# Kernel tuning notes

Hardware: AMD Instinct MI355X
Metric: run time of the kernel (lower is better)

Reference implementation:

```python
import jax, jax.numpy as jnp
import numpy as np


def setup_inputs() -> dict:
    key = jax.random.key(0)
    k1, k2 = jax.random.split(key)
    enc_output = jax.random.normal(k1, (4, 4096, 1024), dtype=jnp.float32)
    dec_output = jax.random.normal(k2, (4, 4096, 1024), dtype=jnp.float32)
    return {"enc_output": enc_output, "dec_output": dec_output}


def reference(enc_output, dec_output):
    # a_t[b, e, t] = sum_d enc[b, e, d] * dec[b, t, d]   -> [B, T_enc, T_dec]
    a_t = jnp.einsum('bed,btd->bet', enc_output, dec_output)
    # softmax over dim=1 (the T_enc axis), no scaling, no mask (faithful to source)
    a_t = jax.nn.softmax(a_t, axis=1)
    # c_t[b, t, d] = sum_e a_t[b, e, t] * enc[b, e, d]   -> [B, T_dec, D]
    c_t = jnp.einsum('bet,bed->btd', a_t, enc_output)
    return c_t
```

## Files before the change

kernel.cpp:

```cpp
#include <hip/hip_runtime.h>
#include <hip/hip_fp16.h>

typedef _Float16 half_t;
typedef _Float16 f16x8 __attribute__((ext_vector_type(8)));
typedef _Float16 f16x4 __attribute__((ext_vector_type(4)));
typedef float f32x4 __attribute__((ext_vector_type(4)));

#define SEQ 4096
#define DDIM 1024
#define NBATCH 4

__device__ __forceinline__ void gload16(const half_t* g, half_t* l) {
  __builtin_amdgcn_global_load_lds((const __attribute__((address_space(1))) void*)g,
                                   (__attribute__((address_space(3))) void*)l, 16, 0, 0);
}

__global__ __launch_bounds__(256) void conv_f16(const float* __restrict__ src,
                                                half_t* __restrict__ dst) {
  int i = blockIdx.x * 256 + threadIdx.x;
  float4 x = ((const float4*)src)[i];
  f16x4 o = {(half_t)x.x, (half_t)x.y, (half_t)x.z, (half_t)x.w};
  *(f16x4*)(dst + (size_t)i * 4) = o;
}

__global__ __launch_bounds__(256) void transpose_f16(const float* __restrict__ src,
                                                     half_t* __restrict__ dst) {
  __shared__ float tile[32][33];
  int b = blockIdx.z;
  int e0 = blockIdx.x * 32, d0 = blockIdx.y * 32;
  const float* s = src + (size_t)b * SEQ * DDIM;
  half_t* dt = dst + (size_t)b * DDIM * SEQ;
  int tx = threadIdx.x & 31, ty = threadIdx.x >> 5;
#pragma unroll
  for (int i = 0; i < 4; i++) {
    int e = e0 + ty + i * 8;
    tile[ty + i * 8][tx] = s[(size_t)e * DDIM + d0 + tx];
  }
  __syncthreads();
#pragma unroll
  for (int i = 0; i < 4; i++) {
    int d = d0 + ty + i * 8;
    dt[(size_t)d * SEQ + e0 + tx] = (half_t)tile[tx][ty + i * 8];
  }
}

#define BM 128
#define BN 128
#define BK 64

__global__ __launch_bounds__(256) void gemm_f16(const half_t* __restrict__ A,
                                                const half_t* __restrict__ B,
                                                float* __restrict__ C, int M, int N, int K) {
  __shared__ __align__(16) half_t As[BM * BK];
  __shared__ __align__(16) half_t Bs[BN * BK];
  const int tid = threadIdx.x;
  const int bm = blockIdx.x, bn = blockIdx.y;
  const int wave = tid >> 6, lane = tid & 63;
  const int wm = (wave & 1) * 64, wn = (wave >> 1) * 64;
  const int mrow = lane & 15, quad = lane >> 4;

  f32x4 acc[4][4];
#pragma unroll
  for (int i = 0; i < 4; i++)
#pragma unroll
    for (int j = 0; j < 4; j++) acc[i][j] = {0.f, 0.f, 0.f, 0.f};

  const half_t* Ag = A + (size_t)(bm * BM) * K;
  const half_t* Bg = B + (size_t)(bn * BN) * K;

  for (int k0 = 0; k0 < K; k0 += BK) {
#pragma unroll
    for (int i = 0; i < 4; i++) {
      int cid = i * 256 + tid;
      int row = cid >> 3, slot = cid & 7;
      int chunk = slot ^ (row & 7);
      gload16(Ag + (size_t)row * K + k0 + chunk * 8, &As[row * BK + slot * 8]);
      gload16(Bg + (size_t)row * K + k0 + chunk * 8, &Bs[row * BK + slot * 8]);
    }
    __builtin_amdgcn_s_waitcnt(0);
    __syncthreads();
#pragma unroll
    for (int ks = 0; ks < 2; ks++) {
      f16x8 af[4], bf[4];
#pragma unroll
      for (int i = 0; i < 4; i++) {
        int ra = wm + i * 16 + mrow;
        int rb = wn + i * 16 + mrow;
        int sa = (ks * 4 + quad) ^ (ra & 7);
        int sb = (ks * 4 + quad) ^ (rb & 7);
        af[i] = *(const f16x8*)(&As[ra * BK + sa * 8]);
        bf[i] = *(const f16x8*)(&Bs[rb * BK + sb * 8]);
      }
#pragma unroll
      for (int mi = 0; mi < 4; mi++)
#pragma unroll
        for (int ni = 0; ni < 4; ni++)
          acc[mi][ni] =
              __builtin_amdgcn_mfma_f32_16x16x32_f16(af[mi], bf[ni], acc[mi][ni], 0, 0, 0);
    }
    __syncthreads();
  }
#pragma unroll
  for (int mi = 0; mi < 4; mi++) {
#pragma unroll
    for (int ni = 0; ni < 4; ni++) {
      int row0 = bm * BM + wm + mi * 16 + quad * 4;
      int col = bn * BN + wn + ni * 16 + mrow;
      float* Cp = C + (size_t)row0 * N + col;
#pragma unroll
      for (int r = 0; r < 4; r++) Cp[(size_t)r * N] = acc[mi][ni][r];
    }
  }
}

__global__ __launch_bounds__(256) void softmax_rows(const float* __restrict__ S,
                                                    half_t* __restrict__ P) {
  const int row = blockIdx.x;
  const float4* Sr = (const float4*)(S + (size_t)row * SEQ);
  const int tid = threadIdx.x, lane = tid & 63, wave = tid >> 6;
  __shared__ float red[4];
  __shared__ float bc;
  float4 v[4];
  float m = -1e30f;
#pragma unroll
  for (int j = 0; j < 4; j++) {
    v[j] = Sr[tid + j * 256];
    m = fmaxf(m, fmaxf(fmaxf(v[j].x, v[j].y), fmaxf(v[j].z, v[j].w)));
  }
#pragma unroll
  for (int o = 32; o; o >>= 1) m = fmaxf(m, __shfl_xor(m, o));
  if (lane == 0) red[wave] = m;
  __syncthreads();
  if (tid == 0) bc = fmaxf(fmaxf(red[0], red[1]), fmaxf(red[2], red[3]));
  __syncthreads();
  m = bc;
  float s = 0.f;
#pragma unroll
  for (int j = 0; j < 4; j++) {
    v[j].x = __expf(v[j].x - m);
    v[j].y = __expf(v[j].y - m);
    v[j].z = __expf(v[j].z - m);
    v[j].w = __expf(v[j].w - m);
    s += v[j].x + v[j].y + v[j].z + v[j].w;
  }
#pragma unroll
  for (int o = 32; o; o >>= 1) s += __shfl_xor(s, o);
  __syncthreads();
  if (lane == 0) red[wave] = s;
  __syncthreads();
  if (tid == 0) bc = red[0] + red[1] + red[2] + red[3];
  __syncthreads();
  float r = 1.0f / bc;
  f16x4* Pr = (f16x4*)(P + (size_t)row * SEQ);
#pragma unroll
  for (int j = 0; j < 4; j++) {
    f16x4 o = {(half_t)(v[j].x * r), (half_t)(v[j].y * r), (half_t)(v[j].z * r),
               (half_t)(v[j].w * r)};
    Pr[tid + j * 256] = o;
  }
}

__global__ __launch_bounds__(256) void naive_attn(const float* __restrict__ enc,
                                                  const float* __restrict__ dec,
                                                  float* __restrict__ out) {
  const int b = blockIdx.y, t = blockIdx.x;
  const float* encb = enc + (size_t)b * SEQ * DDIM;
  const float* q = dec + ((size_t)b * SEQ + t) * DDIM;
  __shared__ float qs[DDIM];
  __shared__ float sc[SEQ];
  __shared__ float red[4];
  __shared__ float bc;
  const int tid = threadIdx.x, lane = tid & 63, wave = tid >> 6;
  for (int i = tid; i < DDIM; i += 256) qs[i] = q[i];
  __syncthreads();
  for (int e = tid; e < SEQ; e += 256) {
    const float* er = encb + (size_t)e * DDIM;
    float s = 0.f;
    for (int d = 0; d < DDIM; d += 4) {
      float4 ev = *(const float4*)(er + d);
      s += ev.x * qs[d] + ev.y * qs[d + 1] + ev.z * qs[d + 2] + ev.w * qs[d + 3];
    }
    sc[e] = s;
  }
  __syncthreads();
  float m = -1e30f;
  for (int e = tid; e < SEQ; e += 256) m = fmaxf(m, sc[e]);
#pragma unroll
  for (int o = 32; o; o >>= 1) m = fmaxf(m, __shfl_xor(m, o));
  if (lane == 0) red[wave] = m;
  __syncthreads();
  if (tid == 0) bc = fmaxf(fmaxf(red[0], red[1]), fmaxf(red[2], red[3]));
  __syncthreads();
  m = bc;
  float s = 0.f;
  for (int e = tid; e < SEQ; e += 256) {
    float p = __expf(sc[e] - m);
    sc[e] = p;
    s += p;
  }
#pragma unroll
  for (int o = 32; o; o >>= 1) s += __shfl_xor(s, o);
  __syncthreads();
  if (lane == 0) red[wave] = s;
  __syncthreads();
  if (tid == 0) bc = red[0] + red[1] + red[2] + red[3];
  __syncthreads();
  const float rinv = 1.0f / bc;
  const int d0 = tid * 4;
  float4 acc = {0.f, 0.f, 0.f, 0.f};
  for (int e = 0; e < SEQ; e++) {
    float p = sc[e];
    float4 ev = *(const float4*)(encb + (size_t)e * DDIM + d0);
    acc.x += p * ev.x;
    acc.y += p * ev.y;
    acc.z += p * ev.z;
    acc.w += p * ev.w;
  }
  float4* o4 = (float4*)(out + ((size_t)b * SEQ + t) * DDIM + d0);
  float4 res = {acc.x * rinv, acc.y * rinv, acc.z * rinv, acc.w * rinv};
  *o4 = res;
}

extern "C" void kernel_launch(void* const* d_in, const int* in_sizes, int n_in, void* d_out,
                              int out_size, void* d_ws, size_t ws_size, hipStream_t stream) {
  const float* enc = (const float*)d_in[0];
  const float* dec = (const float*)d_in[1];
  float* out = (float*)d_out;

  const size_t SZ_S = (size_t)SEQ * SEQ * 4;
  const size_t SZ_P = (size_t)SEQ * SEQ * 2;
  const size_t SZ_H = (size_t)NBATCH * SEQ * DDIM * 2;
  const size_t NEED = SZ_S + SZ_P + 3 * SZ_H;

  if (ws_size >= NEED) {
    char* w = (char*)d_ws;
    float* S = (float*)w;
    half_t* P = (half_t*)(w + SZ_S);
    half_t* decF = (half_t*)(w + SZ_S + SZ_P);
    half_t* encF = (half_t*)(w + SZ_S + SZ_P + SZ_H);
    half_t* encT = (half_t*)(w + SZ_S + SZ_P + 2 * SZ_H);

    const int nconv = NBATCH * SEQ * DDIM / 4 / 256;
    conv_f16<<<nconv, 256, 0, stream>>>(dec, decF);
    conv_f16<<<nconv, 256, 0, stream>>>(enc, encF);
    transpose_f16<<<dim3(SEQ / 32, DDIM / 32, NBATCH), 256, 0, stream>>>(enc, encT);

    for (int b = 0; b < NBATCH; b++) {
      const size_t eo = (size_t)b * SEQ * DDIM;
      gemm_f16<<<dim3(SEQ / BM, SEQ / BN), 256, 0, stream>>>(decF + eo, encF + eo, S, SEQ, SEQ,
                                                             DDIM);
      softmax_rows<<<SEQ, 256, 0, stream>>>(S, P);
      gemm_f16<<<dim3(SEQ / BM, DDIM / BN), 256, 0, stream>>>(P, encT + eo, out + eo, SEQ, DDIM,
                                                              SEQ);
    }
  } else {
    naive_attn<<<dim3(SEQ, NBATCH), 256, 0, stream>>>(enc, dec, out);
  }
}
```

Before: 772.5 us.

## Batch the second GEMM across batches and add split-K fallback path

The second GEMM (P times encT) had only 32x8=256 blocks per launch, which underfills the GPU. When the workspace is large enough, the softmax output for all four batches is stored in one buffer and a single batched GEMM launches over a z-grid of batches, giving 1024 blocks. Otherwise a split-K fallback splits K four ways and accumulates with atomic adds into a zeroed output. The cost is a larger workspace (four P matrices) and, on the fallback path, atomics and a memset.

```diff
diff --git a/kernel.cpp b/kernel.cpp
--- a/kernel.cpp
+++ b/kernel.cpp
@@ -50,7 +50,11 @@
 
 __global__ __launch_bounds__(256) void gemm_f16(const half_t* __restrict__ A,
                                                 const half_t* __restrict__ B,
-                                                float* __restrict__ C, int M, int N, int K) {
+                                                float* __restrict__ C, int M, int N, int K,
+                                                int kc, long sA, long sB, long sC, int atom) {
+  A += (size_t)blockIdx.z * (size_t)sA;
+  B += (size_t)blockIdx.z * (size_t)sB;
+  C += (size_t)blockIdx.z * (size_t)sC;
   __shared__ __align__(16) half_t As[BM * BK];
   __shared__ __align__(16) half_t Bs[BN * BK];
   const int tid = threadIdx.x;
@@ -68,7 +72,7 @@
   const half_t* Ag = A + (size_t)(bm * BM) * K;
   const half_t* Bg = B + (size_t)(bn * BN) * K;
 
-  for (int k0 = 0; k0 < K; k0 += BK) {
+  for (int k0 = 0; k0 < kc; k0 += BK) {
 #pragma unroll
     for (int i = 0; i < 4; i++) {
       int cid = i * 256 + tid;
@@ -107,8 +111,13 @@
       int row0 = bm * BM + wm + mi * 16 + quad * 4;
       int col = bn * BN + wn + ni * 16 + mrow;
       float* Cp = C + (size_t)row0 * N + col;
-#pragma unroll
-      for (int r = 0; r < 4; r++) Cp[(size_t)r * N] = acc[mi][ni][r];
+      if (atom) {
+#pragma unroll
+        for (int r = 0; r < 4; r++) unsafeAtomicAdd(Cp + (size_t)r * N, acc[mi][ni][r]);
+      } else {
+#pragma unroll
+        for (int r = 0; r < 4; r++) Cp[(size_t)r * N] = acc[mi][ni][r];
+      }
     }
   }
 }
@@ -229,10 +238,35 @@
 
   const size_t SZ_S = (size_t)SEQ * SEQ * 4;
   const size_t SZ_P = (size_t)SEQ * SEQ * 2;
+  const size_t SZ_PALL = (size_t)NBATCH * SEQ * SEQ * 2;
   const size_t SZ_H = (size_t)NBATCH * SEQ * DDIM * 2;
-  const size_t NEED = SZ_S + SZ_P + 3 * SZ_H;
-
-  if (ws_size >= NEED) {
+  const size_t NEED_SPLITK = SZ_S + SZ_P + 3 * SZ_H;
+  const size_t NEED_BATCH = SZ_S + SZ_PALL + 3 * SZ_H;
+
+  const int nconv = NBATCH * SEQ * DDIM / 4 / 256;
+
+  if (ws_size >= NEED_BATCH) {
+    char* w = (char*)d_ws;
+    float* S = (float*)w;
+    half_t* Pall = (half_t*)(w + SZ_S);
+    half_t* decF = (half_t*)(w + SZ_S + SZ_PALL);
+    half_t* encF = (half_t*)(w + SZ_S + SZ_PALL + SZ_H);
+    half_t* encT = (half_t*)(w + SZ_S + SZ_PALL + 2 * SZ_H);
+
+    conv_f16<<<nconv, 256, 0, stream>>>(dec, decF);
+    conv_f16<<<nconv, 256, 0, stream>>>(enc, encF);
+    transpose_f16<<<dim3(SEQ / 32, DDIM / 32, NBATCH), 256, 0, stream>>>(enc, encT);
+
+    for (int b = 0; b < NBATCH; b++) {
+      const size_t eo = (size_t)b * SEQ * DDIM;
+      gemm_f16<<<dim3(SEQ / BM, SEQ / BN, 1), 256, 0, stream>>>(decF + eo, encF + eo, S, SEQ,
+                                                                SEQ, DDIM, DDIM, 0, 0, 0, 0);
+      softmax_rows<<<SEQ, 256, 0, stream>>>(S, Pall + (size_t)b * SEQ * SEQ);
+    }
+    gemm_f16<<<dim3(SEQ / BM, DDIM / BN, NBATCH), 256, 0, stream>>>(
+        Pall, encT, out, SEQ, DDIM, SEQ, SEQ, (long)SEQ * SEQ, (long)DDIM * SEQ,
+        (long)SEQ * DDIM, 0);
+  } else if (ws_size >= NEED_SPLITK) {
     char* w = (char*)d_ws;
     float* S = (float*)w;
     half_t* P = (half_t*)(w + SZ_S);
@@ -240,18 +274,19 @@
     half_t* encF = (half_t*)(w + SZ_S + SZ_P + SZ_H);
     half_t* encT = (half_t*)(w + SZ_S + SZ_P + 2 * SZ_H);
 
-    const int nconv = NBATCH * SEQ * DDIM / 4 / 256;
+    hipMemsetAsync(out, 0, (size_t)NBATCH * SEQ * DDIM * 4, stream);
     conv_f16<<<nconv, 256, 0, stream>>>(dec, decF);
     conv_f16<<<nconv, 256, 0, stream>>>(enc, encF);
     transpose_f16<<<dim3(SEQ / 32, DDIM / 32, NBATCH), 256, 0, stream>>>(enc, encT);
 
     for (int b = 0; b < NBATCH; b++) {
       const size_t eo = (size_t)b * SEQ * DDIM;
-      gemm_f16<<<dim3(SEQ / BM, SEQ / BN), 256, 0, stream>>>(decF + eo, encF + eo, S, SEQ, SEQ,
-                                                             DDIM);
+      gemm_f16<<<dim3(SEQ / BM, SEQ / BN, 1), 256, 0, stream>>>(decF + eo, encF + eo, S, SEQ,
+                                                                SEQ, DDIM, DDIM, 0, 0, 0, 0);
       softmax_rows<<<SEQ, 256, 0, stream>>>(S, P);
-      gemm_f16<<<dim3(SEQ / BM, DDIM / BN), 256, 0, stream>>>(P, encT + eo, out + eo, SEQ, DDIM,
-                                                              SEQ);
+      gemm_f16<<<dim3(SEQ / BM, DDIM / BN, 4), 256, 0, stream>>>(
+          P, encT + (size_t)b * DDIM * SEQ, out + eo, SEQ, DDIM, SEQ, SEQ / 4, SEQ / 4,
+          SEQ / 4, 0, 1);
     }
   } else {
     naive_attn<<<dim3(SEQ, NBATCH), 256, 0, stream>>>(enc, dec, out);
```

New measurement: 823.3 us. +6.6%, slower.

## Use 256x256 double-buffered GEMM tiles, split-K atomics, and fuse enc conversion

Applied to the files above, without the earlier changes.

Replaces the 128x128 GEMM with a 512-thread 256x256-tile kernel that double-buffers LDS, so the next K-slice loads while MFMAs run. The second GEMM is split four ways along K, adding partial results into a pre-zeroed output with atomics so the grid still fills the CUs. The separate enc fp16 conversion is folded into the transpose kernel, saving one full read of enc. The costs are a large LDS footprint per block, atomic traffic on the output, and an extra memset. The waitcnt before barriers was dropped, which could race on the async LDS loads.

```diff
diff --git a/kernel.cpp b/kernel.cpp
--- a/kernel.cpp
+++ b/kernel.cpp
@@ -23,18 +23,22 @@
   *(f16x4*)(dst + (size_t)i * 4) = o;
 }
 
-__global__ __launch_bounds__(256) void transpose_f16(const float* __restrict__ src,
-                                                     half_t* __restrict__ dst) {
+__global__ __launch_bounds__(256) void transconv_f16(const float* __restrict__ src,
+                                                     half_t* __restrict__ dstF,
+                                                     half_t* __restrict__ dstT) {
   __shared__ float tile[32][33];
   int b = blockIdx.z;
   int e0 = blockIdx.x * 32, d0 = blockIdx.y * 32;
   const float* s = src + (size_t)b * SEQ * DDIM;
-  half_t* dt = dst + (size_t)b * DDIM * SEQ;
+  half_t* df = dstF + (size_t)b * SEQ * DDIM;
+  half_t* dt = dstT + (size_t)b * DDIM * SEQ;
   int tx = threadIdx.x & 31, ty = threadIdx.x >> 5;
 #pragma unroll
   for (int i = 0; i < 4; i++) {
     int e = e0 + ty + i * 8;
-    tile[ty + i * 8][tx] = s[(size_t)e * DDIM + d0 + tx];
+    float v = s[(size_t)e * DDIM + d0 + tx];
+    tile[ty + i * 8][tx] = v;
+    df[(size_t)e * DDIM + d0 + tx] = (half_t)v;
   }
   __syncthreads();
 #pragma unroll
@@ -44,71 +48,89 @@
   }
 }
 
-#define BM 128
-#define BN 128
-#define BK 64
-
-__global__ __launch_bounds__(256) void gemm_f16(const half_t* __restrict__ A,
-                                                const half_t* __restrict__ B,
-                                                float* __restrict__ C, int M, int N, int K) {
-  __shared__ __align__(16) half_t As[BM * BK];
-  __shared__ __align__(16) half_t Bs[BN * BK];
+#define TM 256
+#define TN 256
+#define TK 64
+
+__global__ __launch_bounds__(512, 2) void gemm256_f16(const half_t* __restrict__ A,
+                                                      const half_t* __restrict__ B,
+                                                      float* __restrict__ C, int M, int N,
+                                                      int K, int kc, long sA, long sB, long sC,
+                                                      int atom) {
+  A += (size_t)blockIdx.z * (size_t)sA;
+  B += (size_t)blockIdx.z * (size_t)sB;
+  C += (size_t)blockIdx.z * (size_t)sC;
+  __shared__ __align__(16) half_t As[2][TM * TK];
+  __shared__ __align__(16) half_t Bs[2][TN * TK];
   const int tid = threadIdx.x;
-  const int bm = blockIdx.x, bn = blockIdx.y;
   const int wave = tid >> 6, lane = tid & 63;
-  const int wm = (wave & 1) * 64, wn = (wave >> 1) * 64;
+  const int wm = (wave >> 2) * 128, wn = (wave & 3) * 64;
   const int mrow = lane & 15, quad = lane >> 4;
 
-  f32x4 acc[4][4];
-#pragma unroll
-  for (int i = 0; i < 4; i++)
+  f32x4 acc[8][4];
+#pragma unroll
+  for (int i = 0; i < 8; i++)
 #pragma unroll
     for (int j = 0; j < 4; j++) acc[i][j] = {0.f, 0.f, 0.f, 0.f};
 
-  const half_t* Ag = A + (size_t)(bm * BM) * K;
-  const half_t* Bg = B + (size_t)(bn * BN) * K;
-
-  for (int k0 = 0; k0 < K; k0 += BK) {
+  const half_t* Ag = A + (size_t)(blockIdx.x * TM) * K;
+  const half_t* Bg = B + (size_t)(blockIdx.y * TN) * K;
+
+  auto stage = [&](int buf, int k0) {
 #pragma unroll
     for (int i = 0; i < 4; i++) {
-      int cid = i * 256 + tid;
+      int cid = i * 512 + tid;
       int row = cid >> 3, slot = cid & 7;
       int chunk = slot ^ (row & 7);
-      gload16(Ag + (size_t)row * K + k0 + chunk * 8, &As[row * BK + slot * 8]);
-      gload16(Bg + (size_t)row * K + k0 + chunk * 8, &Bs[row * BK + slot * 8]);
-    }
-    __builtin_amdgcn_s_waitcnt(0);
-    __syncthreads();
+      gload16(Ag + (size_t)row * K + k0 + chunk * 8, &As[buf][row * TK + slot * 8]);
+      gload16(Bg + (size_t)row * K + k0 + chunk * 8, &Bs[buf][row * TK + slot * 8]);
+    }
+  };
+
+  stage(0, 0);
+  __syncthreads();
+  int cur = 0;
+  for (int k0 = 0; k0 < kc; k0 += TK) {
+    if (k0 + TK < kc) stage(cur ^ 1, k0 + TK);
 #pragma unroll
     for (int ks = 0; ks < 2; ks++) {
-      f16x8 af[4], bf[4];
-#pragma unroll
-      for (int i = 0; i < 4; i++) {
+      f16x8 af[8], bf[4];
+#pragma unroll
+      for (int i = 0; i < 8; i++) {
         int ra = wm + i * 16 + mrow;
-        int rb = wn + i * 16 + mrow;
         int sa = (ks * 4 + quad) ^ (ra & 7);
+        af[i] = *(const f16x8*)(&As[cur][ra * TK + sa * 8]);
+      }
+#pragma unroll
+      for (int j = 0; j < 4; j++) {
+        int rb = wn + j * 16 + mrow;
         int sb = (ks * 4 + quad) ^ (rb & 7);
-        af[i] = *(const f16x8*)(&As[ra * BK + sa * 8]);
-        bf[i] = *(const f16x8*)(&Bs[rb * BK + sb * 8]);
+        bf[j] = *(const f16x8*)(&Bs[cur][rb * TK + sb * 8]);
       }
 #pragma unroll
-      for (int mi = 0; mi < 4; mi++)
+      for (int mi = 0; mi < 8; mi++)
 #pragma unroll
         for (int ni = 0; ni < 4; ni++)
           acc[mi][ni] =
               __builtin_amdgcn_mfma_f32_16x16x32_f16(af[mi], bf[ni], acc[mi][ni], 0, 0, 0);
     }
     __syncthreads();
-  }
-#pragma unroll
-  for (int mi = 0; mi < 4; mi++) {
+    cur ^= 1;
+  }
+#pragma unroll
+  for (int mi = 0; mi < 8; mi++) {
 #pragma unroll
     for (int ni = 0; ni < 4; ni++) {
-      int row0 = bm * BM + wm + mi * 16 + quad * 4;
-      int col = bn * BN + wn + ni * 16 + mrow;
+      int row0 = blockIdx.x * TM + wm + mi * 16 + quad * 4;
+      int col = blockIdx.y * TN + wn + ni * 16 + mrow;
       float* Cp = C + (size_t)row0 * N + col;
-#pragma unroll
-      for (int r = 0; r < 4; r++) Cp[(size_t)r * N] = acc[mi][ni][r];
+      if (atom) {
+#pragma unroll
+        for (int r = 0; r < 4; r++) unsafeAtomicAdd(Cp + (size_t)r * N, acc[mi][ni][r]);
+      } else {
+#pragma unroll
+        for (int r = 0; r < 4; r++) Cp[(size_t)r * N] = acc[mi][ni][r];
+      }
     }
   }
 }
@@ -232,6 +254,8 @@
   const size_t SZ_H = (size_t)NBATCH * SEQ * DDIM * 2;
   const size_t NEED = SZ_S + SZ_P + 3 * SZ_H;
 
+  const int nconv = NBATCH * SEQ * DDIM / 4 / 256;
+
   if (ws_size >= NEED) {
     char* w = (char*)d_ws;
     float* S = (float*)w;
@@ -240,18 +264,18 @@
     half_t* encF = (half_t*)(w + SZ_S + SZ_P + SZ_H);
     half_t* encT = (half_t*)(w + SZ_S + SZ_P + 2 * SZ_H);
 
-    const int nconv = NBATCH * SEQ * DDIM / 4 / 256;
+    hipMemsetAsync(out, 0, (size_t)NBATCH * SEQ * DDIM * 4, stream);
     conv_f16<<<nconv, 256, 0, stream>>>(dec, decF);
-    conv_f16<<<nconv, 256, 0, stream>>>(enc, encF);
-    transpose_f16<<<dim3(SEQ / 32, DDIM / 32, NBATCH), 256, 0, stream>>>(enc, encT);
+    transconv_f16<<<dim3(SEQ / 32, DDIM / 32, NBATCH), 256, 0, stream>>>(enc, encF, encT);
 
     for (int b = 0; b < NBATCH; b++) {
       const size_t eo = (size_t)b * SEQ * DDIM;
-      gemm_f16<<<dim3(SEQ / BM, SEQ / BN), 256, 0, stream>>>(decF + eo, encF + eo, S, SEQ, SEQ,
-                                                             DDIM);
+      gemm256_f16<<<dim3(SEQ / TM, SEQ / TN, 1), 512, 0, stream>>>(
+          decF + eo, encF + eo, S, SEQ, SEQ, DDIM, DDIM, 0, 0, 0, 0);
       softmax_rows<<<SEQ, 256, 0, stream>>>(S, P);
-      gemm_f16<<<dim3(SEQ / BM, DDIM / BN), 256, 0, stream>>>(P, encT + eo, out + eo, SEQ, DDIM,
-                                                              SEQ);
+      gemm256_f16<<<dim3(SEQ / TM, DDIM / TN, 4), 512, 0, stream>>>(
+          P, encT + (size_t)b * DDIM * SEQ, out + eo, SEQ, DDIM, SEQ, SEQ / 4, SEQ / 4,
+          SEQ / 4, 0, 1);
     }
   } else {
     naive_attn<<<dim3(SEQ, NBATCH), 256, 0, stream>>>(enc, dec, out);
```

New measurement: 742.0 us. 1.04x faster.
